# Kernel optimization log

Hardware: AMD Instinct MI355X
Metric: run time of the kernel (lower is better)

Reference implementation:

```python
import jax, jax.numpy as jnp
import numpy as np


def setup_inputs() -> dict:
    key = jax.random.key(0)
    kq, kk, kv = jax.random.split(key, 3)
    B, L, H, E = 2, 4096, 8, 64
    queries = jax.random.normal(kq, (B, L, H, E), dtype=jnp.float32)
    keys = jax.random.normal(kk, (B, L, H, E), dtype=jnp.float32)
    values = jax.random.normal(kv, (B, L, H, E), dtype=jnp.float32)
    return {"queries": queries, "keys": keys, "values": values}


def reference(queries, keys, values):
    # queries: (B, L, H, E); keys: (B, S, H, E); values: (B, S, H, D)
    E = queries.shape[-1]
    scale = 1.0 / jnp.sqrt(jnp.asarray(E, dtype=queries.dtype))
    # Full LxS score matrix, faithful to the original einsum formulation.
    scores = jnp.einsum('blhe,bshe->bhls', queries, keys)  # (B, H, L, S)
    attn = jax.nn.softmax(scale * scores, axis=-1)
    # dropout prob = 0.0 -> identity
    out = jnp.einsum('bhls,bshd->blhd', attn, values)  # (B, L, H, D)
    return out
```

## Files before the change

kernel.cpp:

```cpp
#include <hip/hip_runtime.h>
#include <hip/hip_bf16.h>

typedef __attribute__((ext_vector_type(16))) float f32x16;
typedef __attribute__((ext_vector_type(8)))  short bf16x8;
typedef __attribute__((ext_vector_type(4)))  short short4v;
typedef __attribute__((ext_vector_type(4)))  float float4v;

#define B_  2
#define L_  4096
#define H_  8
#define E_  64
#define HE  (H_*E_)
#define NT  (L_/64)
#define NT2 32

__device__ __forceinline__ short f2bf(float f) {
    unsigned u = __builtin_bit_cast(unsigned, f);
    u += 0x7fffu + ((u >> 16) & 1u);
    return (short)(u >> 16);
}

__device__ __forceinline__ unsigned cvt_pk(float a, float b) {
    unsigned r;
    asm("v_cvt_pk_bf16_f32 %0, %1, %2" : "=v"(r) : "v"(a), "v"(b));
    return r;
}

__device__ __forceinline__ float exp2f_fast(float x) { return __builtin_amdgcn_exp2f(x); }

__device__ __forceinline__ void gll16(const unsigned short* g, unsigned short* lds) {
    __builtin_amdgcn_global_load_lds(
        (const __attribute__((address_space(1))) unsigned int*)g,
        (__attribute__((address_space(3))) unsigned int*)lds,
        16, 0, 0);
}

__global__ __launch_bounds__(256) void prep_kv(
    const float* __restrict__ Kp, const float* __restrict__ Vp,
    unsigned short* __restrict__ wsK, unsigned short* __restrict__ wsV)
{
    const int tid = threadIdx.x;
    int bid = blockIdx.x;
    const bool isV = bid >= 1024;
    if (isV) bid -= 1024;
    const int t  = bid & 63;
    const int bh = bid >> 6;
    const int b  = bh >> 3, h = bh & 7;
    const int kv0 = t * 64;
    const float* base = (isV ? Vp : Kp) + (size_t)b * ((size_t)L_ * HE) + (size_t)h * E_;

    __shared__ __attribute__((aligned(16))) unsigned short tile[64 * 64];

#pragma unroll
    for (int i = 0; i < 4; ++i) {
        int idx = i * 256 + tid;
        int row = idx >> 4;
        int c4  = (idx & 15) * 4;
        float4v v = *reinterpret_cast<const float4v*>(base + (size_t)(kv0 + row) * HE + c4);
        short4v s;
        s[0] = f2bf(v.x); s[1] = f2bf(v.y); s[2] = f2bf(v.z); s[3] = f2bf(v.w);
        *reinterpret_cast<short4v*>(&tile[row * 64 + c4]) = s;
    }
    __syncthreads();

    if (!isV) {
        unsigned short* out = wsK + (size_t)bid * 4096;
#pragma unroll
        for (int i = 0; i < 2; ++i) {
            int cidx = i * 256 + tid;
            int lane = cidx & 63, ks = (cidx >> 6) & 3, sub = cidx >> 8;
            int lo = lane & 31, hi = lane >> 5;
            bf16x8 v = *reinterpret_cast<const bf16x8*>(&tile[(sub * 32 + lo) * 64 + ks * 16 + hi * 8]);
            *reinterpret_cast<bf16x8*>(&out[(size_t)cidx * 8]) = v;
        }
    } else {
        unsigned short* out = wsV + (size_t)bid * 4096;
#pragma unroll
        for (int i = 0; i < 2; ++i) {
            int cidx = i * 256 + tid;
            int lane = cidx & 63, half = (cidx >> 6) & 1, c = cidx >> 7;
            int lo = lane & 31, hi = lane >> 5;
            int d  = lo + 32 * half;
            int r0 = c * 16 + hi * 4;
            bf16x8 v;
#pragma unroll
            for (int j = 0; j < 8; ++j) {
                int row = r0 + (j & 3) + 8 * (j >> 2);
                v[j] = (short)tile[row * 64 + d];
            }
            *reinterpret_cast<bf16x8*>(&out[(size_t)cidx * 8]) = v;
        }
    }
}

__global__ __launch_bounds__(256, 4) void attn_split(
    const float* __restrict__ Qp,
    const unsigned short* __restrict__ wsK, const unsigned short* __restrict__ wsV,
    float* __restrict__ wsO, float* __restrict__ wsL)
{
    const int tid = threadIdx.x;
    const int w   = tid >> 6;
    const int l   = tid & 63;
    const int lo  = l & 31;
    const int hi  = l >> 5;

    const int bid0 = blockIdx.x;
    const int bid  = (bid0 & 7) * 128 + (bid0 >> 3);
    const int s  = bid & 1;
    const int qt = (bid >> 1) & 31;
    const int bh = bid >> 6;
    const int b  = bh >> 3;
    const int h  = bh & 7;
    const int q0 = qt * 128;

    const float* qbase = Qp + (size_t)b * ((size_t)L_ * HE) + (size_t)h * E_;
    const unsigned short* kt_base = wsK + (size_t)bh * ((size_t)NT * 4096) + (size_t)s * NT2 * 4096;
    const unsigned short* vt_base = wsV + (size_t)bh * ((size_t)NT * 4096) + (size_t)s * NT2 * 4096;

    __shared__ __attribute__((aligned(16))) unsigned short K2[2][4096];
    __shared__ __attribute__((aligned(16))) unsigned short V3s[3][4096];

    const int qrow = q0 + w * 32 + lo;
    const float scale2 = 0.125f * 1.44269504088896f;
    bf16x8 qf[4];
#pragma unroll
    for (int ks = 0; ks < 4; ++ks) {
        const float* p = qbase + (size_t)qrow * HE + ks * 16 + hi * 8;
        float4v a = *reinterpret_cast<const float4v*>(p);
        float4v c = *reinterpret_cast<const float4v*>(p + 4);
        bf16x8 q;
        q[0] = f2bf(a.x * scale2); q[1] = f2bf(a.y * scale2);
        q[2] = f2bf(a.z * scale2); q[3] = f2bf(a.w * scale2);
        q[4] = f2bf(c.x * scale2); q[5] = f2bf(c.y * scale2);
        q[6] = f2bf(c.z * scale2); q[7] = f2bf(c.w * scale2);
        qf[ks] = q;
    }

    f32x16 o0, o1;
#pragma unroll
    for (int r = 0; r < 16; ++r) { o0[r] = 0.f; o1[r] = 0.f; }
    float l_run = 0.f;

    auto stage = [&](int kc, int vc, int t) {
        const unsigned short* kt = kt_base + (size_t)t * 4096;
        const unsigned short* vt = vt_base + (size_t)t * 4096;
#pragma unroll
        for (int i = 0; i < 4; ++i) {
            int p = w * 4 + i;
            if (p < 8) gll16(kt + p * 512 + l * 8, &K2[kc][p * 512]);
            else       gll16(vt + (p - 8) * 512 + l * 8, &V3s[vc][(p - 8) * 512]);
        }
    };

    stage(0, 0, 0);
    __syncthreads();

    f32x16 c0, c1;
#pragma unroll
    for (int r = 0; r < 16; ++r) { c0[r] = 0.f; c1[r] = 0.f; }
    {
        const unsigned short* kb = K2[0];
        __builtin_amdgcn_s_setprio(1);
#pragma unroll
        for (int ks = 0; ks < 4; ++ks) {
            bf16x8 k0 = *reinterpret_cast<const bf16x8*>(&kb[(ks * 64 + l) * 8]);
            bf16x8 k1 = *reinterpret_cast<const bf16x8*>(&kb[((4 + ks) * 64 + l) * 8]);
            c0 = __builtin_amdgcn_mfma_f32_32x32x16_bf16(k0, qf[ks], c0, 0, 0, 0);
            c1 = __builtin_amdgcn_mfma_f32_32x32x16_bf16(k1, qf[ks], c1, 0, 0, 0);
        }
        __builtin_amdgcn_s_setprio(0);
    }
    stage(1, 1, 1);

    for (int t = 0; t < NT2; ++t) {
        const bool have_next = (t + 1 < NT2);
        f32x16 n0, n1;
        if (have_next) {
            __syncthreads();
            if (t + 2 < NT2) stage(t & 1, (t + 2) % 3, t + 2);

            const unsigned short* kb = K2[(t + 1) & 1];
#pragma unroll
            for (int r = 0; r < 16; ++r) { n0[r] = 0.f; n1[r] = 0.f; }
            __builtin_amdgcn_s_setprio(1);
#pragma unroll
            for (int ks = 0; ks < 4; ++ks) {
                bf16x8 k0 = *reinterpret_cast<const bf16x8*>(&kb[(ks * 64 + l) * 8]);
                bf16x8 k1 = *reinterpret_cast<const bf16x8*>(&kb[((4 + ks) * 64 + l) * 8]);
                n0 = __builtin_amdgcn_mfma_f32_32x32x16_bf16(k0, qf[ks], n0, 0, 0, 0);
                n1 = __builtin_amdgcn_mfma_f32_32x32x16_bf16(k1, qf[ks], n1, 0, 0, 0);
            }
            __builtin_amdgcn_s_setprio(0);
        }

        float sa = 0.f, sb = 0.f, sc = 0.f, sd = 0.f;
#pragma unroll
        for (int r = 0; r < 8; ++r) {
            c0[r]     = exp2f_fast(c0[r]);     sa += c0[r];
            c0[8 + r] = exp2f_fast(c0[8 + r]); sb += c0[8 + r];
            c1[r]     = exp2f_fast(c1[r]);     sc += c1[r];
            c1[8 + r] = exp2f_fast(c1[8 + r]); sd += c1[8 + r];
        }
        l_run += (sa + sb) + (sc + sd);

        union { bf16x8 v; unsigned u[4]; } pk[4];
#pragma unroll
        for (int q2 = 0; q2 < 4; ++q2) {
            pk[0].u[q2] = cvt_pk(c0[2 * q2],     c0[2 * q2 + 1]);
            pk[1].u[q2] = cvt_pk(c0[8 + 2 * q2], c0[8 + 2 * q2 + 1]);
            pk[2].u[q2] = cvt_pk(c1[2 * q2],     c1[2 * q2 + 1]);
            pk[3].u[q2] = cvt_pk(c1[8 + 2 * q2], c1[8 + 2 * q2 + 1]);
        }

        {
            const unsigned short* vb = V3s[t % 3];
            __builtin_amdgcn_s_setprio(1);
#pragma unroll
            for (int c = 0; c < 4; ++c) {
                bf16x8 vf0 = *reinterpret_cast<const bf16x8*>(&vb[((c * 2 + 0) * 64 + l) * 8]);
                bf16x8 vf1 = *reinterpret_cast<const bf16x8*>(&vb[((c * 2 + 1) * 64 + l) * 8]);
                o0 = __builtin_amdgcn_mfma_f32_32x32x16_bf16(pk[c].v, vf0, o0, 0, 0, 0);
                o1 = __builtin_amdgcn_mfma_f32_32x32x16_bf16(pk[c].v, vf1, o1, 0, 0, 0);
            }
            __builtin_amdgcn_s_setprio(0);
        }

        if (have_next) { c0 = n0; c1 = n1; }
    }

    const float l_tot = l_run + __shfl_xor(l_run, 32);
    float* oP = wsO + (size_t)s * 4194304;
#pragma unroll
    for (int r = 0; r < 16; ++r) {
        int crow = (r & 3) + 8 * (r >> 2) + 4 * hi;
        float* op = oP + ((size_t)(b * L_ + (q0 + w * 32 + crow)) * H_ + h) * E_;
        op[lo]      = o0[r];
        op[32 + lo] = o1[r];
    }
    if (hi == 0) wsL[s * 65536 + bh * 4096 + q0 + w * 32 + lo] = l_tot;
}

__global__ __launch_bounds__(256) void combine2(
    const float* __restrict__ wsO, const float* __restrict__ wsL,
    float* __restrict__ Op)
{
    const int i4 = blockIdx.x * 256 + threadIdx.x;
    const int flat = i4 << 2;
    const int bhq = flat >> 6;
    const int h  = bhq & 7;
    const int bq = bhq >> 3;
    const int q  = bq & (L_ - 1);
    const int b  = bq >> 12;
    const int bh = b * 8 + h;
    const float l0 = wsL[bh * 4096 + q];
    const float l1 = wsL[65536 + bh * 4096 + q];
    const float inv = 1.f / (l0 + l1);
    float4v p0 = *reinterpret_cast<const float4v*>(wsO + flat);
    float4v p1 = *reinterpret_cast<const float4v*>(wsO + 4194304 + flat);
    float4v o;
    o.x = (p0.x + p1.x) * inv;
    o.y = (p0.y + p1.y) * inv;
    o.z = (p0.z + p1.z) * inv;
    o.w = (p0.w + p1.w) * inv;
    *reinterpret_cast<float4v*>(Op + flat) = o;
}

__global__ __launch_bounds__(256) void attn_main(
    const float* __restrict__ Qp,
    const unsigned short* __restrict__ wsK, const unsigned short* __restrict__ wsV,
    float* __restrict__ Op)
{
    const int tid = threadIdx.x;
    const int w   = tid >> 6;
    const int l   = tid & 63;
    const int lo  = l & 31;
    const int hi  = l >> 5;

    const int bid0 = blockIdx.x;
    const int bid  = (bid0 & 7) * 64 + (bid0 >> 3);
    const int qt = bid & 31;
    const int bh = bid >> 5;
    const int b  = bh >> 3;
    const int h  = bh & 7;
    const int q0 = qt * 128;

    const float* qbase = Qp + (size_t)b * ((size_t)L_ * HE) + (size_t)h * E_;
    float*       obase = Op + (size_t)b * ((size_t)L_ * HE) + (size_t)h * E_;
    const unsigned short* kt_base = wsK + (size_t)bh * ((size_t)NT * 4096);
    const unsigned short* vt_base = wsV + (size_t)bh * ((size_t)NT * 4096);

    __shared__ __attribute__((aligned(16))) unsigned short K3[3][4096];
    __shared__ __attribute__((aligned(16))) unsigned short V3[3][4096];

    const int qrow = q0 + w * 32 + lo;
    const float scale2 = 0.125f * 1.44269504088896f;
    bf16x8 qf[4];
#pragma unroll
    for (int ks = 0; ks < 4; ++ks) {
        const float* p = qbase + (size_t)qrow * HE + ks * 16 + hi * 8;
        float4v a = *reinterpret_cast<const float4v*>(p);
        float4v c = *reinterpret_cast<const float4v*>(p + 4);
        bf16x8 q;
        q[0] = f2bf(a.x * scale2); q[1] = f2bf(a.y * scale2);
        q[2] = f2bf(a.z * scale2); q[3] = f2bf(a.w * scale2);
        q[4] = f2bf(c.x * scale2); q[5] = f2bf(c.y * scale2);
        q[6] = f2bf(c.z * scale2); q[7] = f2bf(c.w * scale2);
        qf[ks] = q;
    }

    f32x16 o0, o1;
#pragma unroll
    for (int r = 0; r < 16; ++r) { o0[r] = 0.f; o1[r] = 0.f; }
    float l_run = 0.f;

    auto stage = [&](int c, int t) {
        const unsigned short* kt = kt_base + (size_t)t * 4096;
        const unsigned short* vt = vt_base + (size_t)t * 4096;
#pragma unroll
        for (int i = 0; i < 4; ++i) {
            int p = w * 4 + i;
            if (p < 8) gll16(kt + p * 512 + l * 8, &K3[c][p * 512]);
            else       gll16(vt + (p - 8) * 512 + l * 8, &V3[c][(p - 8) * 512]);
        }
    };

    stage(0, 0);
    __syncthreads();

    f32x16 c0, c1;
#pragma unroll
    for (int r = 0; r < 16; ++r) { c0[r] = 0.f; c1[r] = 0.f; }
    {
        const unsigned short* kb = K3[0];
        __builtin_amdgcn_s_setprio(1);
#pragma unroll
        for (int ks = 0; ks < 4; ++ks) {
            bf16x8 k0 = *reinterpret_cast<const bf16x8*>(&kb[(ks * 64 + l) * 8]);
            bf16x8 k1 = *reinterpret_cast<const bf16x8*>(&kb[((4 + ks) * 64 + l) * 8]);
            c0 = __builtin_amdgcn_mfma_f32_32x32x16_bf16(k0, qf[ks], c0, 0, 0, 0);
            c1 = __builtin_amdgcn_mfma_f32_32x32x16_bf16(k1, qf[ks], c1, 0, 0, 0);
        }
        __builtin_amdgcn_s_setprio(0);
    }
    stage(1, 1);

    int cur = 0;
    for (int t = 0; t < NT; ++t) {
        int nxt = cur + 1; if (nxt == 3) nxt = 0;
        int fre = nxt + 1; if (fre == 3) fre = 0;
        const bool have_next = (t + 1 < NT);

        f32x16 n0, n1;
        if (have_next) {
            __syncthreads();
            if (t + 2 < NT) stage(fre, t + 2);

            const unsigned short* kb = K3[nxt];
#pragma unroll
            for (int r = 0; r < 16; ++r) { n0[r] = 0.f; n1[r] = 0.f; }
            __builtin_amdgcn_s_setprio(1);
#pragma unroll
            for (int ks = 0; ks < 4; ++ks) {
                bf16x8 k0 = *reinterpret_cast<const bf16x8*>(&kb[(ks * 64 + l) * 8]);
                bf16x8 k1 = *reinterpret_cast<const bf16x8*>(&kb[((4 + ks) * 64 + l) * 8]);
                n0 = __builtin_amdgcn_mfma_f32_32x32x16_bf16(k0, qf[ks], n0, 0, 0, 0);
                n1 = __builtin_amdgcn_mfma_f32_32x32x16_bf16(k1, qf[ks], n1, 0, 0, 0);
            }
            __builtin_amdgcn_s_setprio(0);
        }

        float sa = 0.f, sb = 0.f, sc = 0.f, sd = 0.f;
#pragma unroll
        for (int r = 0; r < 8; ++r) {
            c0[r]     = exp2f_fast(c0[r]);     sa += c0[r];
            c0[8 + r] = exp2f_fast(c0[8 + r]); sb += c0[8 + r];
            c1[r]     = exp2f_fast(c1[r]);     sc += c1[r];
            c1[8 + r] = exp2f_fast(c1[8 + r]); sd += c1[8 + r];
        }
        l_run += (sa + sb) + (sc + sd);

        union { bf16x8 v; unsigned u[4]; } pk[4];
#pragma unroll
        for (int q2 = 0; q2 < 4; ++q2) {
            pk[0].u[q2] = cvt_pk(c0[2 * q2],     c0[2 * q2 + 1]);
            pk[1].u[q2] = cvt_pk(c0[8 + 2 * q2], c0[8 + 2 * q2 + 1]);
            pk[2].u[q2] = cvt_pk(c1[2 * q2],     c1[2 * q2 + 1]);
            pk[3].u[q2] = cvt_pk(c1[8 + 2 * q2], c1[8 + 2 * q2 + 1]);
        }

        {
            const unsigned short* vb = V3[cur];
            __builtin_amdgcn_s_setprio(1);
#pragma unroll
            for (int c = 0; c < 4; ++c) {
                bf16x8 vf0 = *reinterpret_cast<const bf16x8*>(&vb[((c * 2 + 0) * 64 + l) * 8]);
                bf16x8 vf1 = *reinterpret_cast<const bf16x8*>(&vb[((c * 2 + 1) * 64 + l) * 8]);
                o0 = __builtin_amdgcn_mfma_f32_32x32x16_bf16(pk[c].v, vf0, o0, 0, 0, 0);
                o1 = __builtin_amdgcn_mfma_f32_32x32x16_bf16(pk[c].v, vf1, o1, 0, 0, 0);
            }
            __builtin_amdgcn_s_setprio(0);
        }

        if (have_next) { c0 = n0; c1 = n1; }
        cur = nxt;
    }

    const float l_tot = l_run + __shfl_xor(l_run, 32);
#pragma unroll
    for (int r = 0; r < 16; ++r) {
        int crow = (r & 3) + 8 * (r >> 2) + 4 * hi;
        float denom = __shfl(l_tot, crow);
        float inv = 1.f / denom;
        float* op = obase + (size_t)(q0 + w * 32 + crow) * HE;
        op[lo]      = o0[r] * inv;
        op[32 + lo] = o1[r] * inv;
    }
}

__global__ __launch_bounds__(256) void attn_fwd_fb(
    const float* __restrict__ Qp, const float* __restrict__ Kp,
    const float* __restrict__ Vp, float* __restrict__ Op)
{
    const int tid = threadIdx.x;
    const int w   = tid >> 6;
    const int l   = tid & 63;
    const int lo  = l & 31;
    const int hi  = l >> 5;
    const int bid0 = blockIdx.x;
    const int bid  = (bid0 & 7) * 64 + (bid0 >> 3);
    const int qt = bid & 31;
    const int bh = bid >> 5;
    const int b  = bh >> 3;
    const int h  = bh & 7;
    const int q0 = qt * 128;

    const size_t head_off = (size_t)b * ((size_t)L_ * HE) + (size_t)h * E_;
    const float* qbase = Qp + head_off;
    const float* kbase = Kp + head_off;
    const float* vbase = Vp + head_off;
    float*       obase = Op + head_off;

    __shared__ __attribute__((aligned(16))) unsigned short K_lds[64 * 64];
    __shared__ __attribute__((aligned(16))) unsigned short VT_lds[64 * 64];

    const int qrow = q0 + w * 32 + lo;
    const float scale = 0.125f;
    bf16x8 qf[4];
#pragma unroll
    for (int ks = 0; ks < 4; ++ks) {
        const float* p = qbase + (size_t)qrow * HE + ks * 16 + hi * 8;
        float4v a = *reinterpret_cast<const float4v*>(p);
        float4v c = *reinterpret_cast<const float4v*>(p + 4);
        bf16x8 q;
        q[0] = f2bf(a.x * scale); q[1] = f2bf(a.y * scale);
        q[2] = f2bf(a.z * scale); q[3] = f2bf(a.w * scale);
        q[4] = f2bf(c.x * scale); q[5] = f2bf(c.y * scale);
        q[6] = f2bf(c.z * scale); q[7] = f2bf(c.w * scale);
        qf[ks] = q;
    }

    f32x16 o0, o1;
#pragma unroll
    for (int r = 0; r < 16; ++r) { o0[r] = 0.f; o1[r] = 0.f; }
    float m_run = -INFINITY;
    float l_run = 0.f;
    const int sw0 = (lo & 7) << 3;

    for (int kv0 = 0; kv0 < L_; kv0 += 64) {
        __syncthreads();
#pragma unroll
        for (int i = 0; i < 4; ++i) {
            int idx = i * 256 + tid;
            int row = idx >> 4;
            int c4  = (idx & 15) * 4;
            const float* p = kbase + (size_t)(kv0 + row) * HE + c4;
            float4v v = *reinterpret_cast<const float4v*>(p);
            short4v s;
            s[0] = f2bf(v.x); s[1] = f2bf(v.y); s[2] = f2bf(v.z); s[3] = f2bf(v.w);
            *reinterpret_cast<short4v*>(&K_lds[row * 64 + (c4 ^ ((row & 7) << 3))]) = s;
        }
#pragma unroll
        for (int i = 0; i < 4; ++i) {
            int kq = i * 4 + w;
            int d  = l;
            const float* p = vbase + (size_t)(kv0 + kq * 4) * HE + d;
            float v0 = p[0 * HE], v1 = p[1 * HE], v2 = p[2 * HE], v3 = p[3 * HE];
            short4v s;
            s[0] = f2bf(v0); s[1] = f2bf(v1); s[2] = f2bf(v2); s[3] = f2bf(v3);
            *reinterpret_cast<short4v*>(&VT_lds[d * 64 + ((kq * 4) ^ ((d & 7) << 3))]) = s;
        }
        __syncthreads();

        f32x16 s0, s1;
#pragma unroll
        for (int r = 0; r < 16; ++r) { s0[r] = 0.f; s1[r] = 0.f; }
#pragma unroll
        for (int ks = 0; ks < 4; ++ks) {
            int ecol = ks * 16 + hi * 8;
            bf16x8 k0 = *reinterpret_cast<const bf16x8*>(&K_lds[lo * 64        + (ecol ^ sw0)]);
            bf16x8 k1 = *reinterpret_cast<const bf16x8*>(&K_lds[(32 + lo) * 64 + (ecol ^ sw0)]);
            s0 = __builtin_amdgcn_mfma_f32_32x32x16_bf16(k0, qf[ks], s0, 0, 0, 0);
            s1 = __builtin_amdgcn_mfma_f32_32x32x16_bf16(k1, qf[ks], s1, 0, 0, 0);
        }

        float mx = s0[0];
#pragma unroll
        for (int r = 1; r < 16; ++r) mx = fmaxf(mx, s0[r]);
#pragma unroll
        for (int r = 0; r < 16; ++r) mx = fmaxf(mx, s1[r]);
        mx = fmaxf(mx, __shfl_xor(mx, 32));
        const float m_new = fmaxf(m_run, mx);
        const float corr  = __expf(m_run - m_new);
        float sum = 0.f;
#pragma unroll
        for (int r = 0; r < 16; ++r) { s0[r] = __expf(s0[r] - m_new); sum += s0[r]; }
#pragma unroll
        for (int r = 0; r < 16; ++r) { s1[r] = __expf(s1[r] - m_new); sum += s1[r]; }
        sum += __shfl_xor(sum, 32);
        l_run = l_run * corr + sum;
        m_run = m_new;

#pragma unroll
        for (int r = 0; r < 16; ++r) {
            int crow = (r & 3) + 8 * (r >> 2) + 4 * hi;
            float cf = __shfl(corr, crow);
            o0[r] *= cf;
            o1[r] *= cf;
        }

        bf16x8 pf[4];
#pragma unroll
        for (int j = 0; j < 8; ++j) {
            pf[0][j] = f2bf(s0[j]);
            pf[1][j] = f2bf(s0[8 + j]);
            pf[2][j] = f2bf(s1[j]);
            pf[3][j] = f2bf(s1[8 + j]);
        }

#pragma unroll
        for (int c = 0; c < 4; ++c) {
            int colb = c * 16 + hi * 4;
            short4v a0 = *reinterpret_cast<const short4v*>(&VT_lds[lo * 64        + ( colb      ^ sw0)]);
            short4v a1 = *reinterpret_cast<const short4v*>(&VT_lds[lo * 64        + ((colb + 8) ^ sw0)]);
            short4v b0 = *reinterpret_cast<const short4v*>(&VT_lds[(32 + lo) * 64 + ( colb      ^ sw0)]);
            short4v b1 = *reinterpret_cast<const short4v*>(&VT_lds[(32 + lo) * 64 + ((colb + 8) ^ sw0)]);
            bf16x8 vf0 = __builtin_shufflevector(a0, a1, 0, 1, 2, 3, 4, 5, 6, 7);
            bf16x8 vf1 = __builtin_shufflevector(b0, b1, 0, 1, 2, 3, 4, 5, 6, 7);
            o0 = __builtin_amdgcn_mfma_f32_32x32x16_bf16(pf[c], vf0, o0, 0, 0, 0);
            o1 = __builtin_amdgcn_mfma_f32_32x32x16_bf16(pf[c], vf1, o1, 0, 0, 0);
        }
    }

#pragma unroll
    for (int r = 0; r < 16; ++r) {
        int crow = (r & 3) + 8 * (r >> 2) + 4 * hi;
        float denom = __shfl(l_run, crow);
        float inv = 1.f / denom;
        float* op = obase + (size_t)(q0 + w * 32 + crow) * HE;
        op[lo]      = o0[r] * inv;
        op[32 + lo] = o1[r] * inv;
    }
}

extern "C" void kernel_launch(void* const* d_in, const int* in_sizes, int n_in,
                              void* d_out, int out_size, void* d_ws, size_t ws_size,
                              hipStream_t stream) {
    (void)in_sizes; (void)n_in; (void)out_size;
    const float* Q = (const float*)d_in[0];
    const float* K = (const float*)d_in[1];
    const float* V = (const float*)d_in[2];
    float* O = (float*)d_out;

    const size_t KV_BYTES   = 16ull * 1024 * 1024;
    const size_t SPLIT_NEED = KV_BYTES + (2ull * 4194304 + 2ull * 65536) * 4;

    if (ws_size >= SPLIT_NEED) {
        unsigned short* wsK = (unsigned short*)d_ws;
        unsigned short* wsV = wsK + 4194304;
        float* wsO = (float*)((char*)d_ws + KV_BYTES);
        float* wsL = wsO + 2ull * 4194304;
        hipLaunchKernelGGL(prep_kv,    dim3(2048), dim3(256), 0, stream, K, V, wsK, wsV);
        hipLaunchKernelGGL(attn_split, dim3(1024), dim3(256), 0, stream, Q, wsK, wsV, wsO, wsL);
        hipLaunchKernelGGL(combine2,   dim3(4096), dim3(256), 0, stream, wsO, wsL, O);
    } else if (ws_size >= KV_BYTES) {
        unsigned short* wsK = (unsigned short*)d_ws;
        unsigned short* wsV = wsK + 4194304;
        hipLaunchKernelGGL(prep_kv,   dim3(2048), dim3(256), 0, stream, K, V, wsK, wsV);
        hipLaunchKernelGGL(attn_main, dim3(512),  dim3(256), 0, stream, Q, wsK, wsV, O);
    } else {
        hipLaunchKernelGGL(attn_fwd_fb, dim3(512), dim3(256), 0, stream, Q, K, V, O);
    }
}
```

Baseline: 116.9 us.

## Replace software-pipelined QK prefetch with simple double-buffered loop

Both attention kernels drop the skewed pipeline, which computed the next tile's QK^T scores while applying softmax and PV to the current tile with triple-buffered LDS. They now use a plain double-buffered loop: stage tile t+1, compute scores, exp, and PV for tile t, then synchronise at the end of the iteration. This cuts LDS use and live registers, since the n0/n1 accumulators are gone, which may let more waves fit per CU. In exchange it loses the overlap between the QK MFMAs and the exp work. The occupancy hint is also removed from attn_split's launch bounds.

```diff
diff --git a/kernel.cpp b/kernel.cpp
--- a/kernel.cpp
+++ b/kernel.cpp
@@ -93,7 +93,7 @@
     }
 }
 
-__global__ __launch_bounds__(256, 4) void attn_split(
+__global__ __launch_bounds__(256) void attn_split(
     const float* __restrict__ Qp,
     const unsigned short* __restrict__ wsK, const unsigned short* __restrict__ wsV,
     float* __restrict__ wsO, float* __restrict__ wsL)
@@ -118,7 +118,7 @@
     const unsigned short* vt_base = wsV + (size_t)bh * ((size_t)NT * 4096) + (size_t)s * NT2 * 4096;
 
     __shared__ __attribute__((aligned(16))) unsigned short K2[2][4096];
-    __shared__ __attribute__((aligned(16))) unsigned short V3s[3][4096];
+    __shared__ __attribute__((aligned(16))) unsigned short V2[2][4096];
 
     const int qrow = q0 + w * 32 + lo;
     const float scale2 = 0.125f * 1.44269504088896f;
@@ -139,93 +139,78 @@
     f32x16 o0, o1;
 #pragma unroll
     for (int r = 0; r < 16; ++r) { o0[r] = 0.f; o1[r] = 0.f; }
+    f32x16 Zv;
+#pragma unroll
+    for (int r = 0; r < 16; ++r) Zv[r] = 0.f;
     float l_run = 0.f;
 
-    auto stage = [&](int kc, int vc, int t) {
+    auto stage = [&](int c, int t) {
         const unsigned short* kt = kt_base + (size_t)t * 4096;
         const unsigned short* vt = vt_base + (size_t)t * 4096;
 #pragma unroll
         for (int i = 0; i < 4; ++i) {
             int p = w * 4 + i;
-            if (p < 8) gll16(kt + p * 512 + l * 8, &K2[kc][p * 512]);
-            else       gll16(vt + (p - 8) * 512 + l * 8, &V3s[vc][(p - 8) * 512]);
+            if (p < 8) gll16(kt + p * 512 + l * 8, &K2[c][p * 512]);
+            else       gll16(vt + (p - 8) * 512 + l * 8, &V2[c][(p - 8) * 512]);
         }
     };
 
-    stage(0, 0, 0);
+    stage(0, 0);
     __syncthreads();
 
-    f32x16 c0, c1;
-#pragma unroll
-    for (int r = 0; r < 16; ++r) { c0[r] = 0.f; c1[r] = 0.f; }
-    {
-        const unsigned short* kb = K2[0];
+    for (int t = 0; t < NT2; ++t) {
+        const int p = t & 1;
+        if (t + 1 < NT2) stage(p ^ 1, t + 1);
+
+        const unsigned short* kb = K2[p];
+        f32x16 s0, s1;
         __builtin_amdgcn_s_setprio(1);
-#pragma unroll
-        for (int ks = 0; ks < 4; ++ks) {
+        {
+            bf16x8 k0 = *reinterpret_cast<const bf16x8*>(&kb[(0 * 64 + l) * 8]);
+            bf16x8 k1 = *reinterpret_cast<const bf16x8*>(&kb[(4 * 64 + l) * 8]);
+            s0 = __builtin_amdgcn_mfma_f32_32x32x16_bf16(k0, qf[0], Zv, 0, 0, 0);
+            s1 = __builtin_amdgcn_mfma_f32_32x32x16_bf16(k1, qf[0], Zv, 0, 0, 0);
+        }
+#pragma unroll
+        for (int ks = 1; ks < 4; ++ks) {
             bf16x8 k0 = *reinterpret_cast<const bf16x8*>(&kb[(ks * 64 + l) * 8]);
             bf16x8 k1 = *reinterpret_cast<const bf16x8*>(&kb[((4 + ks) * 64 + l) * 8]);
-            c0 = __builtin_amdgcn_mfma_f32_32x32x16_bf16(k0, qf[ks], c0, 0, 0, 0);
-            c1 = __builtin_amdgcn_mfma_f32_32x32x16_bf16(k1, qf[ks], c1, 0, 0, 0);
+            s0 = __builtin_amdgcn_mfma_f32_32x32x16_bf16(k0, qf[ks], s0, 0, 0, 0);
+            s1 = __builtin_amdgcn_mfma_f32_32x32x16_bf16(k1, qf[ks], s1, 0, 0, 0);
         }
         __builtin_amdgcn_s_setprio(0);
-    }
-    stage(1, 1, 1);
-
-    for (int t = 0; t < NT2; ++t) {
-        const bool have_next = (t + 1 < NT2);
-        f32x16 n0, n1;
-        if (have_next) {
-            __syncthreads();
-            if (t + 2 < NT2) stage(t & 1, (t + 2) % 3, t + 2);
-
-            const unsigned short* kb = K2[(t + 1) & 1];
-#pragma unroll
-            for (int r = 0; r < 16; ++r) { n0[r] = 0.f; n1[r] = 0.f; }
-            __builtin_amdgcn_s_setprio(1);
-#pragma unroll
-            for (int ks = 0; ks < 4; ++ks) {
-                bf16x8 k0 = *reinterpret_cast<const bf16x8*>(&kb[(ks * 64 + l) * 8]);
-                bf16x8 k1 = *reinterpret_cast<const bf16x8*>(&kb[((4 + ks) * 64 + l) * 8]);
-                n0 = __builtin_amdgcn_mfma_f32_32x32x16_bf16(k0, qf[ks], n0, 0, 0, 0);
-                n1 = __builtin_amdgcn_mfma_f32_32x32x16_bf16(k1, qf[ks], n1, 0, 0, 0);
-            }
-            __builtin_amdgcn_s_setprio(0);
-        }
 
         float sa = 0.f, sb = 0.f, sc = 0.f, sd = 0.f;
 #pragma unroll
         for (int r = 0; r < 8; ++r) {
-            c0[r]     = exp2f_fast(c0[r]);     sa += c0[r];
-            c0[8 + r] = exp2f_fast(c0[8 + r]); sb += c0[8 + r];
-            c1[r]     = exp2f_fast(c1[r]);     sc += c1[r];
-            c1[8 + r] = exp2f_fast(c1[8 + r]); sd += c1[8 + r];
+            s0[r]     = exp2f_fast(s0[r]);     sa += s0[r];
+            s0[8 + r] = exp2f_fast(s0[8 + r]); sb += s0[8 + r];
+            s1[r]     = exp2f_fast(s1[r]);     sc += s1[r];
+            s1[8 + r] = exp2f_fast(s1[8 + r]); sd += s1[8 + r];
         }
         l_run += (sa + sb) + (sc + sd);
 
         union { bf16x8 v; unsigned u[4]; } pk[4];
 #pragma unroll
         for (int q2 = 0; q2 < 4; ++q2) {
-            pk[0].u[q2] = cvt_pk(c0[2 * q2],     c0[2 * q2 + 1]);
-            pk[1].u[q2] = cvt_pk(c0[8 + 2 * q2], c0[8 + 2 * q2 + 1]);
-            pk[2].u[q2] = cvt_pk(c1[2 * q2],     c1[2 * q2 + 1]);
-            pk[3].u[q2] = cvt_pk(c1[8 + 2 * q2], c1[8 + 2 * q2 + 1]);
-        }
-
-        {
-            const unsigned short* vb = V3s[t % 3];
-            __builtin_amdgcn_s_setprio(1);
-#pragma unroll
-            for (int c = 0; c < 4; ++c) {
-                bf16x8 vf0 = *reinterpret_cast<const bf16x8*>(&vb[((c * 2 + 0) * 64 + l) * 8]);
-                bf16x8 vf1 = *reinterpret_cast<const bf16x8*>(&vb[((c * 2 + 1) * 64 + l) * 8]);
-                o0 = __builtin_amdgcn_mfma_f32_32x32x16_bf16(pk[c].v, vf0, o0, 0, 0, 0);
-                o1 = __builtin_amdgcn_mfma_f32_32x32x16_bf16(pk[c].v, vf1, o1, 0, 0, 0);
-            }
-            __builtin_amdgcn_s_setprio(0);
-        }
-
-        if (have_next) { c0 = n0; c1 = n1; }
+            pk[0].u[q2] = cvt_pk(s0[2 * q2],     s0[2 * q2 + 1]);
+            pk[1].u[q2] = cvt_pk(s0[8 + 2 * q2], s0[8 + 2 * q2 + 1]);
+            pk[2].u[q2] = cvt_pk(s1[2 * q2],     s1[2 * q2 + 1]);
+            pk[3].u[q2] = cvt_pk(s1[8 + 2 * q2], s1[8 + 2 * q2 + 1]);
+        }
+
+        const unsigned short* vb = V2[p];
+        __builtin_amdgcn_s_setprio(1);
+#pragma unroll
+        for (int c = 0; c < 4; ++c) {
+            bf16x8 vf0 = *reinterpret_cast<const bf16x8*>(&vb[((c * 2 + 0) * 64 + l) * 8]);
+            bf16x8 vf1 = *reinterpret_cast<const bf16x8*>(&vb[((c * 2 + 1) * 64 + l) * 8]);
+            o0 = __builtin_amdgcn_mfma_f32_32x32x16_bf16(pk[c].v, vf0, o0, 0, 0, 0);
+            o1 = __builtin_amdgcn_mfma_f32_32x32x16_bf16(pk[c].v, vf1, o1, 0, 0, 0);
+        }
+        __builtin_amdgcn_s_setprio(0);
+
+        __syncthreads();
     }
 
     const float l_tot = l_run + __shfl_xor(l_run, 32);
@@ -289,8 +274,8 @@
     const unsigned short* kt_base = wsK + (size_t)bh * ((size_t)NT * 4096);
     const unsigned short* vt_base = wsV + (size_t)bh * ((size_t)NT * 4096);
 
-    __shared__ __attribute__((aligned(16))) unsigned short K3[3][4096];
-    __shared__ __attribute__((aligned(16))) unsigned short V3[3][4096];
+    __shared__ __attribute__((aligned(16))) unsigned short K2[2][4096];
+    __shared__ __attribute__((aligned(16))) unsigned short V2[2][4096];
 
     const int qrow = q0 + w * 32 + lo;
     const float scale2 = 0.125f * 1.44269504088896f;
@@ -311,6 +296,9 @@
     f32x16 o0, o1;
 #pragma unroll
     for (int r = 0; r < 16; ++r) { o0[r] = 0.f; o1[r] = 0.f; }
+    f32x16 Zv;
+#pragma unroll
+    for (int r = 0; r < 16; ++r) Zv[r] = 0.f;
     float l_run = 0.f;
 
     auto stage = [&](int c, int t) {
@@ -319,90 +307,67 @@
 #pragma unroll
         for (int i = 0; i < 4; ++i) {
             int p = w * 4 + i;
-            if (p < 8) gll16(kt + p * 512 + l * 8, &K3[c][p * 512]);
-            else       gll16(vt + (p - 8) * 512 + l * 8, &V3[c][(p - 8) * 512]);
+            if (p < 8) gll16(kt + p * 512 + l * 8, &K2[c][p * 512]);
+            else       gll16(vt + (p - 8) * 512 + l * 8, &V2[c][(p - 8) * 512]);
         }
     };
 
     stage(0, 0);
     __syncthreads();
 
-    f32x16 c0, c1;
-#pragma unroll
-    for (int r = 0; r < 16; ++r) { c0[r] = 0.f; c1[r] = 0.f; }
-    {
-        const unsigned short* kb = K3[0];
+    for (int t = 0; t < NT; ++t) {
+        const int p = t & 1;
+        if (t + 1 < NT) stage(p ^ 1, t + 1);
+
+        const unsigned short* kb = K2[p];
+        f32x16 s0, s1;
         __builtin_amdgcn_s_setprio(1);
-#pragma unroll
-        for (int ks = 0; ks < 4; ++ks) {
+        {
+            bf16x8 k0 = *reinterpret_cast<const bf16x8*>(&kb[(0 * 64 + l) * 8]);
+            bf16x8 k1 = *reinterpret_cast<const bf16x8*>(&kb[(4 * 64 + l) * 8]);
+            s0 = __builtin_amdgcn_mfma_f32_32x32x16_bf16(k0, qf[0], Zv, 0, 0, 0);
+            s1 = __builtin_amdgcn_mfma_f32_32x32x16_bf16(k1, qf[0], Zv, 0, 0, 0);
+        }
+#pragma unroll
+        for (int ks = 1; ks < 4; ++ks) {
             bf16x8 k0 = *reinterpret_cast<const bf16x8*>(&kb[(ks * 64 + l) * 8]);
             bf16x8 k1 = *reinterpret_cast<const bf16x8*>(&kb[((4 + ks) * 64 + l) * 8]);
-            c0 = __builtin_amdgcn_mfma_f32_32x32x16_bf16(k0, qf[ks], c0, 0, 0, 0);
-            c1 = __builtin_amdgcn_mfma_f32_32x32x16_bf16(k1, qf[ks], c1, 0, 0, 0);
+            s0 = __builtin_amdgcn_mfma_f32_32x32x16_bf16(k0, qf[ks], s0, 0, 0, 0);
+            s1 = __builtin_amdgcn_mfma_f32_32x32x16_bf16(k1, qf[ks], s1, 0, 0, 0);
         }
         __builtin_amdgcn_s_setprio(0);
-    }
-    stage(1, 1);
-
-    int cur = 0;
-    for (int t = 0; t < NT; ++t) {
-        int nxt = cur + 1; if (nxt == 3) nxt = 0;
-        int fre = nxt + 1; if (fre == 3) fre = 0;
-        const bool have_next = (t + 1 < NT);
-
-        f32x16 n0, n1;
-        if (have_next) {
-            __syncthreads();
-            if (t + 2 < NT) stage(fre, t + 2);
-
-            const unsigned short* kb = K3[nxt];
-#pragma unroll
-            for (int r = 0; r < 16; ++r) { n0[r] = 0.f; n1[r] = 0.f; }
-            __builtin_amdgcn_s_setprio(1);
-#pragma unroll
-            for (int ks = 0; ks < 4; ++ks) {
-                bf16x8 k0 = *reinterpret_cast<const bf16x8*>(&kb[(ks * 64 + l) * 8]);
-                bf16x8 k1 = *reinterpret_cast<const bf16x8*>(&kb[((4 + ks) * 64 + l) * 8]);
-                n0 = __builtin_amdgcn_mfma_f32_32x32x16_bf16(k0, qf[ks], n0, 0, 0, 0);
-                n1 = __builtin_amdgcn_mfma_f32_32x32x16_bf16(k1, qf[ks], n1, 0, 0, 0);
-            }
-            __builtin_amdgcn_s_setprio(0);
-        }
 
         float sa = 0.f, sb = 0.f, sc = 0.f, sd = 0.f;
 #pragma unroll
         for (int r = 0; r < 8; ++r) {
-            c0[r]     = exp2f_fast(c0[r]);     sa += c0[r];
-            c0[8 + r] = exp2f_fast(c0[8 + r]); sb += c0[8 + r];
-            c1[r]     = exp2f_fast(c1[r]);     sc += c1[r];
-            c1[8 + r] = exp2f_fast(c1[8 + r]); sd += c1[8 + r];
+            s0[r]     = exp2f_fast(s0[r]);     sa += s0[r];
+            s0[8 + r] = exp2f_fast(s0[8 + r]); sb += s0[8 + r];
+            s1[r]     = exp2f_fast(s1[r]);     sc += s1[r];
+            s1[8 + r] = exp2f_fast(s1[8 + r]); sd += s1[8 + r];
         }
         l_run += (sa + sb) + (sc + sd);
 
         union { bf16x8 v; unsigned u[4]; } pk[4];
 #pragma unroll
         for (int q2 = 0; q2 < 4; ++q2) {
-            pk[0].u[q2] = cvt_pk(c0[2 * q2],     c0[2 * q2 + 1]);
-            pk[1].u[q2] = cvt_pk(c0[8 + 2 * q2], c0[8 + 2 * q2 + 1]);
-            pk[2].u[q2] = cvt_pk(c1[2 * q2],     c1[2 * q2 + 1]);
-            pk[3].u[q2] = cvt_pk(c1[8 + 2 * q2], c1[8 + 2 * q2 + 1]);
-        }
-
-        {
-            const unsigned short* vb = V3[cur];
-            __builtin_amdgcn_s_setprio(1);
-#pragma unroll
-            for (int c = 0; c < 4; ++c) {
-                bf16x8 vf0 = *reinterpret_cast<const bf16x8*>(&vb[((c * 2 + 0) * 64 + l) * 8]);
-                bf16x8 vf1 = *reinterpret_cast<const bf16x8*>(&vb[((c * 2 + 1) * 64 + l) * 8]);
-                o0 = __builtin_amdgcn_mfma_f32_32x32x16_bf16(pk[c].v, vf0, o0, 0, 0, 0);
-                o1 = __builtin_amdgcn_mfma_f32_32x32x16_bf16(pk[c].v, vf1, o1, 0, 0, 0);
-            }
-            __builtin_amdgcn_s_setprio(0);
-        }
-
-        if (have_next) { c0 = n0; c1 = n1; }
-        cur = nxt;
+            pk[0].u[q2] = cvt_pk(s0[2 * q2],     s0[2 * q2 + 1]);
+            pk[1].u[q2] = cvt_pk(s0[8 + 2 * q2], s0[8 + 2 * q2 + 1]);
+            pk[2].u[q2] = cvt_pk(s1[2 * q2],     s1[2 * q2 + 1]);
+            pk[3].u[q2] = cvt_pk(s1[8 + 2 * q2], s1[8 + 2 * q2 + 1]);
+        }
+
+        const unsigned short* vb = V2[p];
+        __builtin_amdgcn_s_setprio(1);
+#pragma unroll
+        for (int c = 0; c < 4; ++c) {
+            bf16x8 vf0 = *reinterpret_cast<const bf16x8*>(&vb[((c * 2 + 0) * 64 + l) * 8]);
+            bf16x8 vf1 = *reinterpret_cast<const bf16x8*>(&vb[((c * 2 + 1) * 64 + l) * 8]);
+            o0 = __builtin_amdgcn_mfma_f32_32x32x16_bf16(pk[c].v, vf0, o0, 0, 0, 0);
+            o1 = __builtin_amdgcn_mfma_f32_32x32x16_bf16(pk[c].v, vf1, o1, 0, 0, 0);
+        }
+        __builtin_amdgcn_s_setprio(0);
+
+        __syncthreads();
     }
 
     const float l_tot = l_run + __shfl_xor(l_run, 32);
```

After: 114.2 us. 1.02x faster.
